# Kernel tuning notes

Hardware: AMD Instinct MI355X
Metric: run time of the kernel (lower is better)

The kernel has to match this reference:

```python
import jax, jax.numpy as jnp
import numpy as np

IN_CHANNELS = 256


def setup_inputs() -> dict:
    key = jax.random.key(0)
    k0, k1, k2, k3 = jax.random.split(key, 4)
    N, C = 8192, IN_CHANNELS
    x = jax.random.normal(k0, (N, C), dtype=jnp.float32)
    # nn.Linear(C, C, bias=False): y = x @ W.T, W is [out, in] = [C, C]
    s = 1.0 / np.sqrt(C)
    Wq = jax.random.uniform(k1, (C, C), dtype=jnp.float32, minval=-s, maxval=s)
    Wk = jax.random.uniform(k2, (C, C), dtype=jnp.float32, minval=-s, maxval=s)
    Wv = jax.random.uniform(k3, (C, C), dtype=jnp.float32, minval=-s, maxval=s)
    return {"x": x, "Wq": Wq, "Wk": Wk, "Wv": Wv}


def reference(x, Wq, Wk, Wv):
    C = x.shape[-1]
    q = x @ Wq.T  # [N, C]
    k = x @ Wk.T  # [N, C]
    v = x @ Wv.T  # [N, C]
    scores = (q @ k.T) / jnp.sqrt(jnp.asarray(C, dtype=x.dtype))  # [N, N]
    attn = jax.nn.softmax(scores, axis=-1)
    return attn @ v  # [N, C]
```

## Files before the change

kernel.cpp:

```cpp
#include <hip/hip_runtime.h>
#include <hip/hip_bf16.h>


typedef short short8 __attribute__((ext_vector_type(8)));
typedef float f32x4 __attribute__((ext_vector_type(4)));
typedef float f32x16 __attribute__((ext_vector_type(16)));
typedef unsigned int u32x4 __attribute__((ext_vector_type(4)));

#define AS1 __attribute__((address_space(1)))
#define AS3 __attribute__((address_space(3)))

static __device__ __forceinline__ void gl_lds16(const void* g, void* l) {
    __builtin_amdgcn_global_load_lds((const AS1 unsigned int*)g,
                                     (AS3 unsigned int*)l, 16, 0, 0);
}

static __device__ __forceinline__ unsigned short f2bf(float f) {
    __hip_bfloat16 h = __float2bfloat16(f);
    return __builtin_bit_cast(unsigned short, h);
}
static __device__ __forceinline__ float bf2f(unsigned short u) {
    unsigned x = ((unsigned)u) << 16;
    return __builtin_bit_cast(float, x);
}
static __device__ __forceinline__ float exp2_fast(float x) {
    float r; asm("v_exp_f32 %0, %1" : "=v"(r) : "v"(x)); return r;
}
static __device__ __forceinline__ unsigned cvt_pk_bf16(float lo, float hi) {
    unsigned r;
    asm("v_cvt_pk_bf16_f32 %0, %1, %2" : "=v"(r) : "v"(lo), "v"(hi));
    return r;
}

static __device__ __forceinline__ short8 pack8(float4 a, float4 b) {
    short8 v;
    v[0] = (short)f2bf(a.x); v[1] = (short)f2bf(a.y);
    v[2] = (short)f2bf(a.z); v[3] = (short)f2bf(a.w);
    v[4] = (short)f2bf(b.x); v[5] = (short)f2bf(b.y);
    v[6] = (short)f2bf(b.z); v[7] = (short)f2bf(b.w);
    return v;
}

__global__ __launch_bounds__(256) void proj_kernel(
    const float* __restrict__ x, const float* __restrict__ Wq,
    const float* __restrict__ Wk, const float* __restrict__ Wv,
    unsigned short* __restrict__ qb, unsigned short* __restrict__ kbt,
    unsigned short* __restrict__ vtc)
{
    const int mb = blockIdx.x, nb = blockIdx.y;
    __shared__ unsigned short xs[64 * 256];
    __shared__ unsigned short wsh[64 * 256];
    const int tid = threadIdx.x;
    const int wid = tid >> 6, lane = tid & 63;
    const int l15 = lane & 15, kg = lane >> 4;

    for (int i = 0; i < 8; ++i) {
        int id = i * 256 + tid;
        int r = id >> 5, c = id & 31;
        {
            const float* g = x + (size_t)(mb * 64 + r) * 256 + c * 8;
            float4 f0 = *(const float4*)g, f1 = *(const float4*)(g + 4);
            *(short8*)&xs[r * 256 + ((c ^ (r & 7)) * 8)] = pack8(f0, f1);
        }
        {
            const float* g = Wq + (size_t)(nb * 64 + r) * 256 + c * 8;
            float4 f0 = *(const float4*)g, f1 = *(const float4*)(g + 4);
            *(short8*)&wsh[r * 256 + ((c ^ (r & 7)) * 8)] = pack8(f0, f1);
        }
    }
    __syncthreads();

    const int arow = wid * 16 + l15;
    short8 a[8];
#pragma unroll
    for (int ks = 0; ks < 8; ++ks)
        a[ks] = *(const short8*)&xs[arow * 256 + (((ks * 4 + kg) ^ (arow & 7)) * 8)];

    for (int w = 0; w < 3; ++w) {
        const float scale = (w == 0) ? 0.09016844005555f : 1.0f;
#pragma unroll
        for (int nt = 0; nt < 4; ++nt) {
            f32x4 acc = {0.f, 0.f, 0.f, 0.f};
            const int brow = nt * 16 + l15;
#pragma unroll
            for (int ks = 0; ks < 8; ++ks) {
                short8 b = *(const short8*)&wsh[brow * 256 + (((ks * 4 + kg) ^ (brow & 7)) * 8)];
                acc = __builtin_amdgcn_mfma_f32_16x16x32_bf16(a[ks], b, acc, 0, 0, 0);
            }
            const int gcol = nb * 64 + nt * 16 + l15;
#pragma unroll
            for (int r = 0; r < 4; ++r) {
                const int grow = mb * 64 + wid * 16 + kg * 4 + r;
                unsigned short h = f2bf(acc[r] * scale);
                if (w == 0) {
                    qb[(size_t)grow * 256 + gcol] = h;
                } else if (w == 1) {
                    kbt[(size_t)(grow >> 6) * 16384 + (gcol >> 3) * 512
                        + (grow & 63) * 8 + (gcol & 7)] = h;
                } else {
                    vtc[(size_t)(grow >> 3) * 2048 + (size_t)gcol * 8 + (grow & 7)] = h;
                }
            }
        }
        if (w < 2) {
            __syncthreads();
            const float* Wn = (w == 0) ? Wk : Wv;
            for (int i = 0; i < 8; ++i) {
                int id = i * 256 + tid;
                int r = id >> 5, c = id & 31;
                const float* g = Wn + (size_t)(nb * 64 + r) * 256 + c * 8;
                float4 f0 = *(const float4*)g, f1 = *(const float4*)(g + 4);
                *(short8*)&wsh[r * 256 + ((c ^ (r & 7)) * 8)] = pack8(f0, f1);
            }
            __syncthreads();
        }
    }
}

__global__ __launch_bounds__(512, 1) void attn_kernel(
    const unsigned short* __restrict__ qb, const unsigned short* __restrict__ kbt,
    const unsigned short* __restrict__ vtc,
    unsigned short* __restrict__ Opart, float* __restrict__ Lpart)
{
    __shared__ unsigned short Ks[2][32 * 64 * 8];
    __shared__ unsigned short Vs[2][8 * 256 * 8];
    const int bid = blockIdx.x;
    const int split = bid & 7, qblk = bid >> 3;
    const int tid = threadIdx.x, wid = tid >> 6, lane = tid & 63;
    const int l31 = lane & 31, hi = lane >> 5;
    const int qrow0 = qblk * 256 + wid * 32;

    short8 qf[16];
#pragma unroll
    for (int s = 0; s < 16; ++s)
        qf[s] = *(const short8*)(qb + (size_t)(qrow0 + l31) * 256 + s * 16 + hi * 8);

    f32x16 accO[8];
#pragma unroll
    for (int i = 0; i < 8; ++i) accO[i] = (f32x16)(0.f);
    f32x16 lacc = (f32x16)(0.f);

    const int kbase_e = hi * 512 + l31 * 8;
    const int vbase_e = hi * 2048 + l31 * 8;

    auto stage = [&](int t, int b) {
        const size_t g = (size_t)(split * 16 + t);
        const unsigned short* ksrc = kbt + g * 16384 + lane * 8;
#pragma unroll
        for (int i = 0; i < 4; ++i) {
            const int cc = i * 8 + wid;
            gl_lds16(ksrc + cc * 512, &Ks[b][cc * 512]);
        }
        const size_t kcb = (size_t)(split * 128 + t * 8);
        const unsigned short* vsrc = vtc + kcb * 2048 + lane * 8;
#pragma unroll
        for (int i = 0; i < 4; ++i) {
            const int vi = i * 8 + wid;
            const int cc = vi >> 2, b64 = vi & 3;
            gl_lds16(vsrc + cc * 2048 + b64 * 512, &Vs[b][cc * 2048 + b64 * 512]);
        }
    };

    stage(0, 0);
    asm volatile("s_waitcnt vmcnt(0)" ::: "memory");
    __builtin_amdgcn_sched_barrier(0);
    __builtin_amdgcn_s_barrier();

    for (int t = 0; t < 16; ++t) {
        if (t < 15) stage(t + 1, (t + 1) & 1);

        const unsigned short* Kb = Ks[t & 1];
        const unsigned short* Vb = Vs[t & 1];

        f32x16 s0 = (f32x16)(0.f), s1 = (f32x16)(0.f);
        __builtin_amdgcn_s_setprio(1);
#pragma unroll
        for (int s = 0; s < 16; ++s) {
            short8 kf0 = *(const short8*)&Kb[kbase_e + s * 1024];
            short8 kf1 = *(const short8*)&Kb[kbase_e + s * 1024 + 256];
            s0 = __builtin_amdgcn_mfma_f32_32x32x16_bf16(kf0, qf[s], s0, 0, 0, 0);
            s1 = __builtin_amdgcn_mfma_f32_32x32x16_bf16(kf1, qf[s], s1, 0, 0, 0);
        }
        __builtin_amdgcn_s_setprio(0);

#pragma unroll
        for (int i = 0; i < 16; ++i) {
            s0[i] = exp2_fast(s0[i]);
            s1[i] = exp2_fast(s1[i]);
        }
        lacc = lacc + s0 + s1;

        short8 pa[4];
#pragma unroll
        for (int s = 0; s < 4; ++s) {
            const f32x16& P = (s >> 1) ? s1 : s0;
            const int q0 = 8 * (s & 1);
            unsigned X0 = cvt_pk_bf16(P[q0 + 0], P[q0 + 1]);
            unsigned X1 = cvt_pk_bf16(P[q0 + 2], P[q0 + 3]);
            unsigned Y0 = cvt_pk_bf16(P[q0 + 4], P[q0 + 5]);
            unsigned Y1 = cvt_pk_bf16(P[q0 + 6], P[q0 + 7]);
            asm volatile("v_permlane32_swap_b32 %0, %1" : "+v"(X0), "+v"(Y0));
            asm volatile("v_permlane32_swap_b32 %0, %1" : "+v"(X1), "+v"(Y1));
            u32x4 w = {X0, X1, Y0, Y1};
            pa[s] = __builtin_bit_cast(short8, w);
        }

        __builtin_amdgcn_s_setprio(1);
#pragma unroll
        for (int dt = 0; dt < 8; ++dt) {
            f32x16 acc = accO[dt];
#pragma unroll
            for (int s = 0; s < 4; ++s) {
                short8 vf = *(const short8*)&Vb[vbase_e + s * 4096 + dt * 256];
                acc = __builtin_amdgcn_mfma_f32_32x32x16_bf16(pa[s], vf, acc, 0, 0, 0);
            }
            accO[dt] = acc;
        }
        __builtin_amdgcn_s_setprio(0);

        asm volatile("s_waitcnt vmcnt(0)" ::: "memory");
        __builtin_amdgcn_sched_barrier(0);
        __builtin_amdgcn_s_barrier();
    }

    float lt[8];
#pragma unroll
    for (int i = 0; i < 8; ++i) lt[i] = lacc[i] + lacc[i + 8];
#pragma unroll
    for (int off = 4; off >= 1; off >>= 1)
#pragma unroll
        for (int i = 0; i < 4; ++i)
            if (i < off) lt[i] = lt[i] + lt[i + off];
    const float lrow = lt[0] + __shfl_xor(lt[0], 32);

#pragma unroll
    for (int dt = 0; dt < 8; ++dt) {
        const int d = dt * 32 + l31;
#pragma unroll
        for (int reg = 0; reg < 16; ++reg) {
            const int R = (reg & 3) + 8 * (reg >> 2) + 4 * hi;
            const int grow = qrow0 + R;
            Opart[((size_t)split * 8192 + grow) * 256 + d] = f2bf(accO[dt][reg]);
        }
    }
    if (hi == 0) {
        const int grow = qrow0 + l31;
        Lpart[split * 8192 + grow] = lrow;
    }
}

__global__ __launch_bounds__(256) void combine_kernel(
    const unsigned short* __restrict__ Opart, const float* __restrict__ Lpart,
    float* __restrict__ out)
{
    const int idx = blockIdx.x * 256 + threadIdx.x;
    const int row = idx >> 6;
    const int d = (idx & 63) * 4;
    float denom = 0.f;
#pragma unroll
    for (int s = 0; s < 8; ++s) denom += Lpart[s * 8192 + row];
    const float inv = 1.0f / denom;
    float4 acc = {0.f, 0.f, 0.f, 0.f};
#pragma unroll
    for (int s = 0; s < 8; ++s) {
        const unsigned short* p = Opart + ((size_t)s * 8192 + row) * 256 + d;
        unsigned long long u = *(const unsigned long long*)p;
        acc.x += bf2f((unsigned short)(u       & 0xffff));
        acc.y += bf2f((unsigned short)((u>>16) & 0xffff));
        acc.z += bf2f((unsigned short)((u>>32) & 0xffff));
        acc.w += bf2f((unsigned short)((u>>48) & 0xffff));
    }
    float4 r;
    r.x = acc.x * inv; r.y = acc.y * inv; r.z = acc.z * inv; r.w = acc.w * inv;
    *(float4*)(out + (size_t)row * 256 + d) = r;
}

extern "C" void kernel_launch(void* const* d_in, const int* in_sizes, int n_in,
                              void* d_out, int out_size, void* d_ws, size_t ws_size,
                              hipStream_t stream)
{
    const float* x  = (const float*)d_in[0];
    const float* Wq = (const float*)d_in[1];
    const float* Wk = (const float*)d_in[2];
    const float* Wv = (const float*)d_in[3];
    char* ws = (char*)d_ws;
    unsigned short* qb  = (unsigned short*)(ws);
    unsigned short* kbt = (unsigned short*)(ws + (4u << 20));
    unsigned short* vtc = (unsigned short*)(ws + (8u << 20));
    unsigned short* Opart = (unsigned short*)(ws + (12u << 20));
    float* Lpart = (float*)(ws + (44u << 20));
    float* out = (float*)d_out;

    dim3 gA(128, 4);
    proj_kernel<<<gA, 256, 0, stream>>>(x, Wq, Wk, Wv, qb, kbt, vtc);
    attn_kernel<<<256, 512, 0, stream>>>(qb, kbt, vtc, Opart, Lpart);
    combine_kernel<<<2048, 256, 0, stream>>>(Opart, Lpart, out);
}
```

Before: 91.80 us.

## Software-pipeline PV MFMAs one tile behind QK and exp

Splits K and V staging so each V tile is loaded one iteration later. The P·V MFMAs for the previous tile now run right after the current tile's QK^T MFMAs, so the exp2 and bf16 packing work on the vector ALU can overlap with matrix-core work instead of serializing with it. The row-sum accumulator is also cut from 16 to 8 floats to save registers. In exchange, the packed P fragments stay live across the barrier, an epilogue PV step is added after the loop, and register pressure or occupancy may shift.

```diff
diff --git a/kernel.cpp b/kernel.cpp
--- a/kernel.cpp
+++ b/kernel.cpp
@@ -4,6 +4,7 @@
 
 typedef short short8 __attribute__((ext_vector_type(8)));
 typedef float f32x4 __attribute__((ext_vector_type(4)));
+typedef float f32x8 __attribute__((ext_vector_type(8)));
 typedef float f32x16 __attribute__((ext_vector_type(16)));
 typedef unsigned int u32x4 __attribute__((ext_vector_type(4)));
 
@@ -138,12 +139,12 @@
     f32x16 accO[8];
 #pragma unroll
     for (int i = 0; i < 8; ++i) accO[i] = (f32x16)(0.f);
-    f32x16 lacc = (f32x16)(0.f);
+    f32x8 lacc = (f32x8)(0.f);
 
     const int kbase_e = hi * 512 + l31 * 8;
     const int vbase_e = hi * 2048 + l31 * 8;
 
-    auto stage = [&](int t, int b) {
+    auto stageK = [&](int t, int b) {
         const size_t g = (size_t)(split * 16 + t);
         const unsigned short* ksrc = kbt + g * 16384 + lane * 8;
 #pragma unroll
@@ -151,6 +152,8 @@
             const int cc = i * 8 + wid;
             gl_lds16(ksrc + cc * 512, &Ks[b][cc * 512]);
         }
+    };
+    auto stageV = [&](int t, int b) {
         const size_t kcb = (size_t)(split * 128 + t * 8);
         const unsigned short* vsrc = vtc + kcb * 2048 + lane * 8;
 #pragma unroll
@@ -161,16 +164,18 @@
         }
     };
 
-    stage(0, 0);
+    stageK(0, 0);
     asm volatile("s_waitcnt vmcnt(0)" ::: "memory");
     __builtin_amdgcn_sched_barrier(0);
     __builtin_amdgcn_s_barrier();
 
+    short8 paO[4];
+
     for (int t = 0; t < 16; ++t) {
-        if (t < 15) stage(t + 1, (t + 1) & 1);
+        if (t < 15) stageK(t + 1, (t + 1) & 1);
+        stageV(t, t & 1);
 
         const unsigned short* Kb = Ks[t & 1];
-        const unsigned short* Vb = Vs[t & 1];
 
         f32x16 s0 = (f32x16)(0.f), s1 = (f32x16)(0.f);
         __builtin_amdgcn_s_setprio(1);
@@ -183,14 +188,28 @@
         }
         __builtin_amdgcn_s_setprio(0);
 
+        if (t > 0) {
+            const unsigned short* Vb = Vs[(t - 1) & 1];
+#pragma unroll
+            for (int dt = 0; dt < 8; ++dt) {
+                f32x16 acc = accO[dt];
+#pragma unroll
+                for (int s = 0; s < 4; ++s) {
+                    short8 vf = *(const short8*)&Vb[vbase_e + s * 4096 + dt * 256];
+                    acc = __builtin_amdgcn_mfma_f32_32x32x16_bf16(paO[s], vf, acc, 0, 0, 0);
+                }
+                accO[dt] = acc;
+            }
+        }
+
 #pragma unroll
         for (int i = 0; i < 16; ++i) {
             s0[i] = exp2_fast(s0[i]);
             s1[i] = exp2_fast(s1[i]);
         }
-        lacc = lacc + s0 + s1;
-
-        short8 pa[4];
+#pragma unroll
+        for (int i = 0; i < 8; ++i)
+            lacc[i] += (s0[i] + s0[i + 8]) + (s1[i] + s1[i + 8]);
 #pragma unroll
         for (int s = 0; s < 4; ++s) {
             const f32x16& P = (s >> 1) ? s1 : s0;
@@ -202,30 +221,31 @@
             asm volatile("v_permlane32_swap_b32 %0, %1" : "+v"(X0), "+v"(Y0));
             asm volatile("v_permlane32_swap_b32 %0, %1" : "+v"(X1), "+v"(Y1));
             u32x4 w = {X0, X1, Y0, Y1};
-            pa[s] = __builtin_bit_cast(short8, w);
-        }
-
-        __builtin_amdgcn_s_setprio(1);
-#pragma unroll
-        for (int dt = 0; dt < 8; ++dt) {
-            f32x16 acc = accO[dt];
-#pragma unroll
-            for (int s = 0; s < 4; ++s) {
-                short8 vf = *(const short8*)&Vb[vbase_e + s * 4096 + dt * 256];
-                acc = __builtin_amdgcn_mfma_f32_32x32x16_bf16(pa[s], vf, acc, 0, 0, 0);
-            }
-            accO[dt] = acc;
-        }
-        __builtin_amdgcn_s_setprio(0);
+            paO[s] = __builtin_bit_cast(short8, w);
+        }
 
         asm volatile("s_waitcnt vmcnt(0)" ::: "memory");
         __builtin_amdgcn_sched_barrier(0);
         __builtin_amdgcn_s_barrier();
     }
 
+    {
+        const unsigned short* Vb = Vs[15 & 1];
+#pragma unroll
+        for (int dt = 0; dt < 8; ++dt) {
+            f32x16 acc = accO[dt];
+#pragma unroll
+            for (int s = 0; s < 4; ++s) {
+                short8 vf = *(const short8*)&Vb[vbase_e + s * 4096 + dt * 256];
+                acc = __builtin_amdgcn_mfma_f32_32x32x16_bf16(paO[s], vf, acc, 0, 0, 0);
+            }
+            accO[dt] = acc;
+        }
+    }
+
     float lt[8];
 #pragma unroll
-    for (int i = 0; i < 8; ++i) lt[i] = lacc[i] + lacc[i + 8];
+    for (int i = 0; i < 8; ++i) lt[i] = lacc[i];
 #pragma unroll
     for (int off = 4; off >= 1; off >>= 1)
 #pragma unroll
```

Result: no change. 93.14 us (+1.5%).

## Give each attention wave two 32-row query tiles sharing K/V fragments

Applied to the files above, without the earlier changes.

The attention block drops from 8 to 4 waves, and each wave now processes 64 query rows as two 32-row tiles. Every K and V fragment read from LDS feeds two MFMAs, which halves LDS read traffic per unit of compute. The setprio hints are removed and the staging loops are adjusted to 4 waves. Register pressure roughly doubles (two sets of Q fragments and two accumulators of 128 floats each), which risks spills. Fewer waves per CU also means less latency hiding.

```diff
diff --git a/kernel.cpp b/kernel.cpp
--- a/kernel.cpp
+++ b/kernel.cpp
@@ -4,6 +4,7 @@
 
 typedef short short8 __attribute__((ext_vector_type(8)));
 typedef float f32x4 __attribute__((ext_vector_type(4)));
+typedef float f32x8 __attribute__((ext_vector_type(8)));
 typedef float f32x16 __attribute__((ext_vector_type(16)));
 typedef unsigned int u32x4 __attribute__((ext_vector_type(4)));
 
@@ -117,7 +118,7 @@
     }
 }
 
-__global__ __launch_bounds__(512, 1) void attn_kernel(
+__global__ __launch_bounds__(256, 1) void attn_kernel(
     const unsigned short* __restrict__ qb, const unsigned short* __restrict__ kbt,
     const unsigned short* __restrict__ vtc,
     unsigned short* __restrict__ Opart, float* __restrict__ Lpart)
@@ -128,17 +129,19 @@
     const int split = bid & 7, qblk = bid >> 3;
     const int tid = threadIdx.x, wid = tid >> 6, lane = tid & 63;
     const int l31 = lane & 31, hi = lane >> 5;
-    const int qrow0 = qblk * 256 + wid * 32;
-
-    short8 qf[16];
-#pragma unroll
-    for (int s = 0; s < 16; ++s)
-        qf[s] = *(const short8*)(qb + (size_t)(qrow0 + l31) * 256 + s * 16 + hi * 8);
-
-    f32x16 accO[8];
-#pragma unroll
-    for (int i = 0; i < 8; ++i) accO[i] = (f32x16)(0.f);
-    f32x16 lacc = (f32x16)(0.f);
+    const int qrow0 = qblk * 256 + wid * 64;
+
+    short8 qfA[16], qfB[16];
+#pragma unroll
+    for (int s = 0; s < 16; ++s) {
+        qfA[s] = *(const short8*)(qb + (size_t)(qrow0 + l31) * 256 + s * 16 + hi * 8);
+        qfB[s] = *(const short8*)(qb + (size_t)(qrow0 + 32 + l31) * 256 + s * 16 + hi * 8);
+    }
+
+    f32x16 accA[8], accB[8];
+#pragma unroll
+    for (int i = 0; i < 8; ++i) { accA[i] = (f32x16)(0.f); accB[i] = (f32x16)(0.f); }
+    f32x8 laccA = (f32x8)(0.f), laccB = (f32x8)(0.f);
 
     const int kbase_e = hi * 512 + l31 * 8;
     const int vbase_e = hi * 2048 + l31 * 8;
@@ -147,15 +150,15 @@
         const size_t g = (size_t)(split * 16 + t);
         const unsigned short* ksrc = kbt + g * 16384 + lane * 8;
 #pragma unroll
-        for (int i = 0; i < 4; ++i) {
-            const int cc = i * 8 + wid;
+        for (int i = 0; i < 8; ++i) {
+            const int cc = i * 4 + wid;
             gl_lds16(ksrc + cc * 512, &Ks[b][cc * 512]);
         }
         const size_t kcb = (size_t)(split * 128 + t * 8);
         const unsigned short* vsrc = vtc + kcb * 2048 + lane * 8;
 #pragma unroll
-        for (int i = 0; i < 4; ++i) {
-            const int vi = i * 8 + wid;
+        for (int i = 0; i < 8; ++i) {
+            const int vi = i * 4 + wid;
             const int cc = vi >> 2, b64 = vi & 3;
             gl_lds16(vsrc + cc * 2048 + b64 * 512, &Vs[b][cc * 2048 + b64 * 512]);
         }
@@ -172,66 +175,80 @@
         const unsigned short* Kb = Ks[t & 1];
         const unsigned short* Vb = Vs[t & 1];
 
-        f32x16 s0 = (f32x16)(0.f), s1 = (f32x16)(0.f);
-        __builtin_amdgcn_s_setprio(1);
-#pragma unroll
-        for (int s = 0; s < 16; ++s) {
-            short8 kf0 = *(const short8*)&Kb[kbase_e + s * 1024];
-            short8 kf1 = *(const short8*)&Kb[kbase_e + s * 1024 + 256];
-            s0 = __builtin_amdgcn_mfma_f32_32x32x16_bf16(kf0, qf[s], s0, 0, 0, 0);
-            s1 = __builtin_amdgcn_mfma_f32_32x32x16_bf16(kf1, qf[s], s1, 0, 0, 0);
-        }
-        __builtin_amdgcn_s_setprio(0);
-
-#pragma unroll
-        for (int i = 0; i < 16; ++i) {
-            s0[i] = exp2_fast(s0[i]);
-            s1[i] = exp2_fast(s1[i]);
-        }
-        lacc = lacc + s0 + s1;
-
-        short8 pa[4];
-#pragma unroll
-        for (int s = 0; s < 4; ++s) {
-            const f32x16& P = (s >> 1) ? s1 : s0;
-            const int q0 = 8 * (s & 1);
-            unsigned X0 = cvt_pk_bf16(P[q0 + 0], P[q0 + 1]);
-            unsigned X1 = cvt_pk_bf16(P[q0 + 2], P[q0 + 3]);
-            unsigned Y0 = cvt_pk_bf16(P[q0 + 4], P[q0 + 5]);
-            unsigned Y1 = cvt_pk_bf16(P[q0 + 6], P[q0 + 7]);
-            asm volatile("v_permlane32_swap_b32 %0, %1" : "+v"(X0), "+v"(Y0));
-            asm volatile("v_permlane32_swap_b32 %0, %1" : "+v"(X1), "+v"(Y1));
-            u32x4 w = {X0, X1, Y0, Y1};
-            pa[s] = __builtin_bit_cast(short8, w);
-        }
-
-        __builtin_amdgcn_s_setprio(1);
+        short8 paA[4], paB[4];
+
+#pragma unroll
+        for (int sl = 0; sl < 2; ++sl) {
+            f32x16 sA = (f32x16)(0.f), sB = (f32x16)(0.f);
+#pragma unroll
+            for (int s = 0; s < 16; ++s) {
+                short8 kf = *(const short8*)&Kb[kbase_e + s * 1024 + sl * 256];
+                sA = __builtin_amdgcn_mfma_f32_32x32x16_bf16(kf, qfA[s], sA, 0, 0, 0);
+                sB = __builtin_amdgcn_mfma_f32_32x32x16_bf16(kf, qfB[s], sB, 0, 0, 0);
+            }
+#pragma unroll
+            for (int i = 0; i < 16; ++i) {
+                sA[i] = exp2_fast(sA[i]);
+                sB[i] = exp2_fast(sB[i]);
+            }
+#pragma unroll
+            for (int i = 0; i < 8; ++i) {
+                laccA[i] += sA[i] + sA[i + 8];
+                laccB[i] += sB[i] + sB[i + 8];
+            }
+#pragma unroll
+            for (int u = 0; u < 2; ++u) {
+                const int q0 = 8 * u;
+                {
+                    unsigned X0 = cvt_pk_bf16(sA[q0 + 0], sA[q0 + 1]);
+                    unsigned X1 = cvt_pk_bf16(sA[q0 + 2], sA[q0 + 3]);
+                    unsigned Y0 = cvt_pk_bf16(sA[q0 + 4], sA[q0 + 5]);
+                    unsigned Y1 = cvt_pk_bf16(sA[q0 + 6], sA[q0 + 7]);
+                    asm volatile("v_permlane32_swap_b32 %0, %1" : "+v"(X0), "+v"(Y0));
+                    asm volatile("v_permlane32_swap_b32 %0, %1" : "+v"(X1), "+v"(Y1));
+                    u32x4 w = {X0, X1, Y0, Y1};
+                    paA[sl * 2 + u] = __builtin_bit_cast(short8, w);
+                }
+                {
+                    unsigned X0 = cvt_pk_bf16(sB[q0 + 0], sB[q0 + 1]);
+                    unsigned X1 = cvt_pk_bf16(sB[q0 + 2], sB[q0 + 3]);
+                    unsigned Y0 = cvt_pk_bf16(sB[q0 + 4], sB[q0 + 5]);
+                    unsigned Y1 = cvt_pk_bf16(sB[q0 + 6], sB[q0 + 7]);
+                    asm volatile("v_permlane32_swap_b32 %0, %1" : "+v"(X0), "+v"(Y0));
+                    asm volatile("v_permlane32_swap_b32 %0, %1" : "+v"(X1), "+v"(Y1));
+                    u32x4 w = {X0, X1, Y0, Y1};
+                    paB[sl * 2 + u] = __builtin_bit_cast(short8, w);
+                }
+            }
+        }
+
 #pragma unroll
         for (int dt = 0; dt < 8; ++dt) {
-            f32x16 acc = accO[dt];
+            f32x16 aA = accA[dt], aB = accB[dt];
 #pragma unroll
             for (int s = 0; s < 4; ++s) {
                 short8 vf = *(const short8*)&Vb[vbase_e + s * 4096 + dt * 256];
-                acc = __builtin_amdgcn_mfma_f32_32x32x16_bf16(pa[s], vf, acc, 0, 0, 0);
-            }
-            accO[dt] = acc;
-        }
-        __builtin_amdgcn_s_setprio(0);
+                aA = __builtin_amdgcn_mfma_f32_32x32x16_bf16(paA[s], vf, aA, 0, 0, 0);
+                aB = __builtin_amdgcn_mfma_f32_32x32x16_bf16(paB[s], vf, aB, 0, 0, 0);
+            }
+            accA[dt] = aA; accB[dt] = aB;
+        }
 
         asm volatile("s_waitcnt vmcnt(0)" ::: "memory");
         __builtin_amdgcn_sched_barrier(0);
         __builtin_amdgcn_s_barrier();
     }
 
-    float lt[8];
-#pragma unroll
-    for (int i = 0; i < 8; ++i) lt[i] = lacc[i] + lacc[i + 8];
+    float ltA[8], ltB[8];
+#pragma unroll
+    for (int i = 0; i < 8; ++i) { ltA[i] = laccA[i]; ltB[i] = laccB[i]; }
 #pragma unroll
     for (int off = 4; off >= 1; off >>= 1)
 #pragma unroll
         for (int i = 0; i < 4; ++i)
-            if (i < off) lt[i] = lt[i] + lt[i + off];
-    const float lrow = lt[0] + __shfl_xor(lt[0], 32);
+            if (i < off) { ltA[i] += ltA[i + off]; ltB[i] += ltB[i + off]; }
+    const float lrowA = ltA[0] + __shfl_xor(ltA[0], 32);
+    const float lrowB = ltB[0] + __shfl_xor(ltB[0], 32);
 
 #pragma unroll
     for (int dt = 0; dt < 8; ++dt) {
@@ -239,13 +256,13 @@
 #pragma unroll
         for (int reg = 0; reg < 16; ++reg) {
             const int R = (reg & 3) + 8 * (reg >> 2) + 4 * hi;
-            const int grow = qrow0 + R;
-            Opart[((size_t)split * 8192 + grow) * 256 + d] = f2bf(accO[dt][reg]);
+            Opart[((size_t)split * 8192 + qrow0 + R) * 256 + d] = f2bf(accA[dt][reg]);
+            Opart[((size_t)split * 8192 + qrow0 + 32 + R) * 256 + d] = f2bf(accB[dt][reg]);
         }
     }
     if (hi == 0) {
-        const int grow = qrow0 + l31;
-        Lpart[split * 8192 + grow] = lrow;
+        Lpart[split * 8192 + qrow0 + l31] = lrowA;
+        Lpart[split * 8192 + qrow0 + 32 + l31] = lrowB;
     }
 }
 
@@ -293,6 +310,6 @@
 
     dim3 gA(128, 4);
     proj_kernel<<<gA, 256, 0, stream>>>(x, Wq, Wk, Wv, qb, kbt, vtc);
-    attn_kernel<<<256, 512, 0, stream>>>(qb, kbt, vtc, Opart, Lpart);
+    attn_kernel<<<256, 256, 0, stream>>>(qb, kbt, vtc, Opart, Lpart);
     combine_kernel<<<2048, 256, 0, stream>>>(Opart, Lpart, out);
 }
```

Measured after the change: 205.1 us. 123% more time.

## Shrink attention KV tile to 32 keys and run two 256-thread blocks per CU

Applied to the files above, without the earlier changes.

Each attention block now has 4 waves covering 128 query rows, and the grid doubles to 512 blocks. Each step stages 32 keys instead of 64, with the K layout in the projection kernel regrouped into 32-row chunks to match. The QK^T product splits the head dimension across two accumulators that are summed before exp, so each step runs one 32x32 score tile. The aim is two resident blocks per CU, letting one block's compute overlap the other's waits, at the cost of twice as many loop iterations and barriers and half the reuse of each staged K/V tile.

```diff
diff --git a/kernel.cpp b/kernel.cpp
--- a/kernel.cpp
+++ b/kernel.cpp
@@ -4,6 +4,7 @@
 
 typedef short short8 __attribute__((ext_vector_type(8)));
 typedef float f32x4 __attribute__((ext_vector_type(4)));
+typedef float f32x8 __attribute__((ext_vector_type(8)));
 typedef float f32x16 __attribute__((ext_vector_type(16)));
 typedef unsigned int u32x4 __attribute__((ext_vector_type(4)));
 
@@ -95,8 +96,8 @@
                 if (w == 0) {
                     qb[(size_t)grow * 256 + gcol] = h;
                 } else if (w == 1) {
-                    kbt[(size_t)(grow >> 6) * 16384 + (gcol >> 3) * 512
-                        + (grow & 63) * 8 + (gcol & 7)] = h;
+                    kbt[(size_t)(grow >> 5) * 8192 + (gcol >> 3) * 256
+                        + (grow & 31) * 8 + (gcol & 7)] = h;
                 } else {
                     vtc[(size_t)(grow >> 3) * 2048 + (size_t)gcol * 8 + (grow & 7)] = h;
                 }
@@ -117,18 +118,18 @@
     }
 }
 
-__global__ __launch_bounds__(512, 1) void attn_kernel(
+__global__ __launch_bounds__(256, 2) void attn_kernel(
     const unsigned short* __restrict__ qb, const unsigned short* __restrict__ kbt,
     const unsigned short* __restrict__ vtc,
     unsigned short* __restrict__ Opart, float* __restrict__ Lpart)
 {
-    __shared__ unsigned short Ks[2][32 * 64 * 8];
-    __shared__ unsigned short Vs[2][8 * 256 * 8];
+    __shared__ unsigned short Ks[2][32 * 32 * 8];
+    __shared__ unsigned short Vs[2][4 * 256 * 8];
     const int bid = blockIdx.x;
     const int split = bid & 7, qblk = bid >> 3;
     const int tid = threadIdx.x, wid = tid >> 6, lane = tid & 63;
     const int l31 = lane & 31, hi = lane >> 5;
-    const int qrow0 = qblk * 256 + wid * 32;
+    const int qrow0 = qblk * 128 + wid * 32;
 
     short8 qf[16];
 #pragma unroll
@@ -138,26 +139,25 @@
     f32x16 accO[8];
 #pragma unroll
     for (int i = 0; i < 8; ++i) accO[i] = (f32x16)(0.f);
-    f32x16 lacc = (f32x16)(0.f);
-
-    const int kbase_e = hi * 512 + l31 * 8;
+    f32x8 lacc = (f32x8)(0.f);
+
+    const int kbase_e = hi * 256 + l31 * 8;
     const int vbase_e = hi * 2048 + l31 * 8;
 
     auto stage = [&](int t, int b) {
-        const size_t g = (size_t)(split * 16 + t);
-        const unsigned short* ksrc = kbt + g * 16384 + lane * 8;
+        const size_t g = (size_t)(split * 32 + t);
+        const unsigned short* ksrc = kbt + g * 8192 + lane * 8;
 #pragma unroll
         for (int i = 0; i < 4; ++i) {
-            const int cc = i * 8 + wid;
-            gl_lds16(ksrc + cc * 512, &Ks[b][cc * 512]);
-        }
-        const size_t kcb = (size_t)(split * 128 + t * 8);
+            const int p = i * 4 + wid;
+            gl_lds16(ksrc + p * 512, &Ks[b][p * 512]);
+        }
+        const size_t kcb = (size_t)(split * 128 + t * 4);
         const unsigned short* vsrc = vtc + kcb * 2048 + lane * 8;
 #pragma unroll
         for (int i = 0; i < 4; ++i) {
-            const int vi = i * 8 + wid;
-            const int cc = vi >> 2, b64 = vi & 3;
-            gl_lds16(vsrc + cc * 2048 + b64 * 512, &Vs[b][cc * 2048 + b64 * 512]);
+            const int p = i * 4 + wid;
+            gl_lds16(vsrc + p * 512, &Vs[b][p * 512]);
         }
     };
 
@@ -166,43 +166,41 @@
     __builtin_amdgcn_sched_barrier(0);
     __builtin_amdgcn_s_barrier();
 
-    for (int t = 0; t < 16; ++t) {
-        if (t < 15) stage(t + 1, (t + 1) & 1);
+    for (int t = 0; t < 32; ++t) {
+        if (t < 31) stage(t + 1, (t + 1) & 1);
 
         const unsigned short* Kb = Ks[t & 1];
         const unsigned short* Vb = Vs[t & 1];
 
-        f32x16 s0 = (f32x16)(0.f), s1 = (f32x16)(0.f);
+        f32x16 sa = (f32x16)(0.f), sb = (f32x16)(0.f);
         __builtin_amdgcn_s_setprio(1);
 #pragma unroll
-        for (int s = 0; s < 16; ++s) {
-            short8 kf0 = *(const short8*)&Kb[kbase_e + s * 1024];
-            short8 kf1 = *(const short8*)&Kb[kbase_e + s * 1024 + 256];
-            s0 = __builtin_amdgcn_mfma_f32_32x32x16_bf16(kf0, qf[s], s0, 0, 0, 0);
-            s1 = __builtin_amdgcn_mfma_f32_32x32x16_bf16(kf1, qf[s], s1, 0, 0, 0);
+        for (int s = 0; s < 16; s += 2) {
+            short8 kf0 = *(const short8*)&Kb[kbase_e + s * 512];
+            short8 kf1 = *(const short8*)&Kb[kbase_e + s * 512 + 512];
+            sa = __builtin_amdgcn_mfma_f32_32x32x16_bf16(kf0, qf[s], sa, 0, 0, 0);
+            sb = __builtin_amdgcn_mfma_f32_32x32x16_bf16(kf1, qf[s + 1], sb, 0, 0, 0);
         }
         __builtin_amdgcn_s_setprio(0);
 
-#pragma unroll
-        for (int i = 0; i < 16; ++i) {
-            s0[i] = exp2_fast(s0[i]);
-            s1[i] = exp2_fast(s1[i]);
-        }
-        lacc = lacc + s0 + s1;
-
-        short8 pa[4];
-#pragma unroll
-        for (int s = 0; s < 4; ++s) {
-            const f32x16& P = (s >> 1) ? s1 : s0;
-            const int q0 = 8 * (s & 1);
-            unsigned X0 = cvt_pk_bf16(P[q0 + 0], P[q0 + 1]);
-            unsigned X1 = cvt_pk_bf16(P[q0 + 2], P[q0 + 3]);
-            unsigned Y0 = cvt_pk_bf16(P[q0 + 4], P[q0 + 5]);
-            unsigned Y1 = cvt_pk_bf16(P[q0 + 6], P[q0 + 7]);
+        f32x16 s0;
+#pragma unroll
+        for (int i = 0; i < 16; ++i) s0[i] = exp2_fast(sa[i] + sb[i]);
+#pragma unroll
+        for (int i = 0; i < 8; ++i) lacc[i] += s0[i] + s0[i + 8];
+
+        short8 pa[2];
+#pragma unroll
+        for (int u = 0; u < 2; ++u) {
+            const int q0 = 8 * u;
+            unsigned X0 = cvt_pk_bf16(s0[q0 + 0], s0[q0 + 1]);
+            unsigned X1 = cvt_pk_bf16(s0[q0 + 2], s0[q0 + 3]);
+            unsigned Y0 = cvt_pk_bf16(s0[q0 + 4], s0[q0 + 5]);
+            unsigned Y1 = cvt_pk_bf16(s0[q0 + 6], s0[q0 + 7]);
             asm volatile("v_permlane32_swap_b32 %0, %1" : "+v"(X0), "+v"(Y0));
             asm volatile("v_permlane32_swap_b32 %0, %1" : "+v"(X1), "+v"(Y1));
             u32x4 w = {X0, X1, Y0, Y1};
-            pa[s] = __builtin_bit_cast(short8, w);
+            pa[u] = __builtin_bit_cast(short8, w);
         }
 
         __builtin_amdgcn_s_setprio(1);
@@ -210,9 +208,9 @@
         for (int dt = 0; dt < 8; ++dt) {
             f32x16 acc = accO[dt];
 #pragma unroll
-            for (int s = 0; s < 4; ++s) {
-                short8 vf = *(const short8*)&Vb[vbase_e + s * 4096 + dt * 256];
-                acc = __builtin_amdgcn_mfma_f32_32x32x16_bf16(pa[s], vf, acc, 0, 0, 0);
+            for (int s2 = 0; s2 < 2; ++s2) {
+                short8 vf = *(const short8*)&Vb[vbase_e + s2 * 4096 + dt * 256];
+                acc = __builtin_amdgcn_mfma_f32_32x32x16_bf16(pa[s2], vf, acc, 0, 0, 0);
             }
             accO[dt] = acc;
         }
@@ -225,7 +223,7 @@
 
     float lt[8];
 #pragma unroll
-    for (int i = 0; i < 8; ++i) lt[i] = lacc[i] + lacc[i + 8];
+    for (int i = 0; i < 8; ++i) lt[i] = lacc[i];
 #pragma unroll
     for (int off = 4; off >= 1; off >>= 1)
 #pragma unroll
@@ -293,6 +291,6 @@
 
     dim3 gA(128, 4);
     proj_kernel<<<gA, 256, 0, stream>>>(x, Wq, Wk, Wv, qb, kbt, vtc);
-    attn_kernel<<<256, 512, 0, stream>>>(qb, kbt, vtc, Opart, Lpart);
+    attn_kernel<<<512, 256, 0, stream>>>(qb, kbt, vtc, Opart, Lpart);
     combine_kernel<<<2048, 256, 0, stream>>>(Opart, Lpart, out);
 }
```

New measurement: 94.58 us. 3.0% more time.
